# Kernel optimization log

Hardware: AMD Instinct MI355X
Metric: run time of the kernel (lower is better)

## Reference

```python
import jax, jax.numpy as jnp
import numpy as np

D_EMB, N_HEADS = 1024, 16
D_K = D_EMB // N_HEADS

def setup_inputs() -> dict:
    key = jax.random.key(0)
    ks = jax.random.split(key, 5)
    scale = 0.02
    return {
        "n": jax.random.normal(ks[0], (2, 2048, D_EMB), dtype=jnp.float32),
        "W_q": jax.random.normal(ks[1], (D_EMB, D_EMB), dtype=jnp.float32) * scale,
        "W_k": jax.random.normal(ks[2], (D_EMB, D_EMB), dtype=jnp.float32) * scale,
        "W_v": jax.random.normal(ks[3], (D_EMB, D_EMB), dtype=jnp.float32) * scale,
        "W_o": jax.random.normal(ks[4], (D_EMB, D_EMB), dtype=jnp.float32) * scale,
    }

def reference(n, W_q, W_k, W_v, W_o):
    B, S, _ = n.shape
    # torch Linear(bias=False): y = x @ W.T, W is [out, in]
    def proj(x, W):
        y = jnp.einsum('bsd,ed->bse', x, W)
        return y.reshape(B, S, N_HEADS, D_K).transpose(0, 2, 1, 3)  # [B,H,S,Dk]
    Q, K, V = proj(n, W_q), proj(n, W_k), proj(n, W_v)
    A = jnp.einsum('bhqd,bhkd->bhqk', Q, K) * (D_K ** -0.5)
    A = jnp.clip(A, -5.0, 5.0)
    A = jax.nn.softmax(A, axis=-1)
    ctx = jnp.einsum('bhqk,bhkd->bhqd', A, V)  # [B,H,S,Dk]
    ctx = ctx.transpose(0, 2, 1, 3).reshape(B, S, D_EMB)
    return jnp.einsum('bsd,ed->bse', ctx, W_o)
```

## Files before the change

### kernel.cpp

```cpp
#include <hip/hip_runtime.h>
#include <hip/hip_bf16.h>
#include <stdint.h>

typedef __attribute__((ext_vector_type(4))) float floatx4;
typedef __attribute__((ext_vector_type(8))) short shortx8;
typedef __attribute__((ext_vector_type(4))) unsigned short ushortx4;
typedef __attribute__((ext_vector_type(8))) unsigned short ushortx8;
typedef __attribute__((ext_vector_type(2))) uint32_t uintx2;

#define MFMA16(a, b, c) __builtin_amdgcn_mfma_f32_16x16x32_bf16((a), (b), (c), 0, 0, 0)

__device__ inline unsigned short f2bf(float f) {
    union { float f; uint32_t u; } v; v.f = f;
    uint32_t u = v.u;
    return (unsigned short)((u + 0x7FFFu + ((u >> 16) & 1u)) >> 16);
}

#if defined(__has_builtin) && __has_builtin(__builtin_amdgcn_cvt_pk_bf16_f32)
__device__ inline uint32_t pkbf(float a, float b) {
    auto r = __builtin_amdgcn_cvt_pk_bf16_f32(a, b);
    union { decltype(r) v; uint32_t u; } x; x.v = r; return x.u;
}
#else
__device__ inline uint32_t pkbf(float a, float b) {
    return ((uint32_t)f2bf(b) << 16) | f2bf(a);
}
#endif

#if defined(__has_builtin) && __has_builtin(__builtin_amdgcn_exp2f)
#define EXP2F(x) __builtin_amdgcn_exp2f(x)
#else
#define EXP2F(x) __expf((x) * 0.69314718056f)
#endif

__device__ inline void gl2lds16(const void* g, void* l) {
    __builtin_amdgcn_global_load_lds(
        (const __attribute__((address_space(1))) void*)(uintptr_t)g,
        (__attribute__((address_space(3))) void*)(uintptr_t)l, 16, 0, 0);
}

__global__ void convert_all(const float* __restrict__ n, const float* __restrict__ wq,
                            const float* __restrict__ wk, const float* __restrict__ wv,
                            const float* __restrict__ wo,
                            unsigned short* __restrict__ nb, unsigned short* __restrict__ wqb,
                            unsigned short* __restrict__ wkb, unsigned short* __restrict__ wvb,
                            unsigned short* __restrict__ wob) {
    int i = blockIdx.x * 256 + threadIdx.x;
    const float* src; unsigned short* dst; int off;
    if (i < 1048576) { src = n; dst = nb; off = i; }
    else {
        int j = i - 1048576; int r = j >> 18; int o = j & 262143;
        src = (r == 0) ? wq : (r == 1) ? wk : (r == 2) ? wv : wo;
        dst = (r == 0) ? wqb : (r == 1) ? wkb : (r == 2) ? wvb : wob;
        off = o;
    }
    floatx4 f = ((const floatx4*)src)[off];
    uintx2 u;
    u.x = pkbf(f.x, f.y); u.y = pkbf(f.z, f.w);
    ((uintx2*)dst)[off] = u;
}

__device__ inline void gemm_tile_128(const unsigned short* __restrict__ A,
                                     const unsigned short* __restrict__ B,
                                     unsigned short* sA, unsigned short* sB,
                                     floatx4 acc[4][4]) {
    const int tid = threadIdx.x, w = tid >> 6, l = tid & 63;
    const int c = l & 15, quad = l >> 4;
    const int wm = (w >> 1) * 64, wn = (w & 1) * 64;
    for (int kt = 0; kt < 16; ++kt) {
        #pragma unroll
        for (int r = 0; r < 4; ++r) {
            int row = r * 32 + w * 8 + (l >> 3);
            int cb  = (l & 7) ^ (row & 7);
            gl2lds16(A + row * 1024 + kt * 64 + cb * 8, (char*)sA + r * 4096 + w * 1024 + l * 16);
            gl2lds16(B + row * 1024 + kt * 64 + cb * 8, (char*)sB + r * 4096 + w * 1024 + l * 16);
        }
        __syncthreads();
        #pragma unroll
        for (int ks = 0; ks < 2; ++ks) {
            shortx8 af[4], bfr[4];
            #pragma unroll
            for (int i2 = 0; i2 < 4; ++i2) {
                int ra = wm + i2 * 16 + c;
                af[i2] = *(const shortx8*)((const char*)sA + ra * 128 + (((ks * 4 + quad) ^ (ra & 7)) * 16));
                int rb = wn + i2 * 16 + c;
                bfr[i2] = *(const shortx8*)((const char*)sB + rb * 128 + (((ks * 4 + quad) ^ (rb & 7)) * 16));
            }
            #pragma unroll
            for (int i2 = 0; i2 < 4; ++i2)
                #pragma unroll
                for (int j2 = 0; j2 < 4; ++j2)
                    acc[i2][j2] = MFMA16(af[i2], bfr[j2], acc[i2][j2]);
        }
        __syncthreads();
    }
}

__global__ void gemm_qkv(const unsigned short* __restrict__ nb,
                         const unsigned short* __restrict__ wqb,
                         const unsigned short* __restrict__ wkb,
                         const unsigned short* __restrict__ wvb,
                         unsigned short* __restrict__ Qb, unsigned short* __restrict__ Kb,
                         unsigned short* __restrict__ VTg) {
    __shared__ unsigned short sAB[2 * 128 * 64];
    unsigned short* sA = sAB;
    unsigned short* sB = sAB + 128 * 64;
    const int mt = blockIdx.x, nt = blockIdx.y;
    const int region = nt >> 3, nl0 = (nt & 7) * 128;
    const unsigned short* W = (region == 0) ? wqb : (region == 1) ? wkb : wvb;
    floatx4 acc[4][4] = {};
    gemm_tile_128(nb + mt * 128 * 1024, W + nl0 * 1024, sA, sB, acc);
    const int tid = threadIdx.x, w = tid >> 6, l = tid & 63, c = l & 15, quad = l >> 4;
    const int wm = (w >> 1) * 64, wn = (w & 1) * 64;
    if (region < 2) {
        unsigned short* O = (region == 0) ? Qb : Kb;
        const float sc = (region == 0) ? 0.18033688f : 1.0f;
        #pragma unroll
        for (int i2 = 0; i2 < 4; ++i2)
            #pragma unroll
            for (int j2 = 0; j2 < 4; ++j2)
                #pragma unroll
                for (int r = 0; r < 4; ++r) {
                    int row = wm + i2 * 16 + quad * 4 + r, col = wn + j2 * 16 + c;
                    sAB[row * 128 + col] = f2bf(acc[i2][j2][r] * sc);
                }
        __syncthreads();
        #pragma unroll
        for (int t = 0; t < 8; ++t) {
            int off = t * 4096 + tid * 16;
            int row = off >> 8, colb = off & 255;
            *(ushortx8*)((char*)(O + (mt * 128 + row) * 1024 + nl0) + colb) =
                *(const ushortx8*)((const char*)sAB + off);
        }
    } else {
        const int hh = w & 1, tt = w >> 1;
        char* img = (char*)sAB + (hh * 2 + tt) * 8192;
        #pragma unroll
        for (int i2 = 0; i2 < 4; ++i2)
            #pragma unroll
            for (int j2 = 0; j2 < 4; ++j2) {
                int d = j2 * 16 + c;
                int blk = (i2 >> 1) * 4 + quad;
                int phys = blk ^ (d & 7);
                uintx2 v;
                v.x = pkbf(acc[i2][j2][0], acc[i2][j2][1]);
                v.y = pkbf(acc[i2][j2][2], acc[i2][j2][3]);
                *(uintx2*)(img + d * 128 + phys * 16 + (i2 & 1) * 8) = v;
            }
        __syncthreads();
        const int h0 = (nt & 7) * 2, t0 = mt * 2;
        #pragma unroll
        for (int g = 0; g < 8; ++g) {
            int off = g * 4096 + tid * 16;
            int hsel = off >> 14, within = off & 16383;
            *(ushortx8*)((char*)VTg + (h0 + hsel) * 524288 + t0 * 8192 + within) =
                *(const ushortx8*)((const char*)sAB + off);
        }
    }
}

__global__ void __launch_bounds__(256) gemm_out(const unsigned short* __restrict__ ctx,
                         const unsigned short* __restrict__ wob,
                         float* __restrict__ out) {
    __shared__ unsigned short sA[128 * 64];
    __shared__ unsigned short sB[64 * 64];
    __shared__ float sC[64 * 64];
    const int mt = blockIdx.x, nt = blockIdx.y;
    const unsigned short* A = ctx + mt * 128 * 1024;
    const unsigned short* B = wob + nt * 64 * 1024;
    const int tid = threadIdx.x, w = tid >> 6, l = tid & 63, c = l & 15, quad = l >> 4;
    const int srow = w * 8 + (l >> 3), scb = l & 7;
    floatx4 acc[2][4] = {};
    for (int kt = 0; kt < 16; ++kt) {
        #pragma unroll
        for (int r = 0; r < 4; ++r) {
            int row = r * 32 + srow, cb = scb ^ (row & 7);
            gl2lds16(A + row * 1024 + kt * 64 + cb * 8, (char*)sA + r * 4096 + w * 1024 + l * 16);
        }
        #pragma unroll
        for (int r = 0; r < 2; ++r) {
            int row = r * 32 + srow, cb = scb ^ (row & 7);
            gl2lds16(B + row * 1024 + kt * 64 + cb * 8, (char*)sB + r * 4096 + w * 1024 + l * 16);
        }
        __syncthreads();
        #pragma unroll
        for (int ks = 0; ks < 2; ++ks) {
            shortx8 af[2], bf2[4];
            #pragma unroll
            for (int i2 = 0; i2 < 2; ++i2) {
                int ra = w * 32 + i2 * 16 + c;
                af[i2] = *(const shortx8*)((const char*)sA + ra * 128 + (((ks * 4 + quad) ^ (ra & 7)) * 16));
            }
            #pragma unroll
            for (int j2 = 0; j2 < 4; ++j2) {
                int rb = j2 * 16 + c;
                bf2[j2] = *(const shortx8*)((const char*)sB + rb * 128 + (((ks * 4 + quad) ^ (rb & 7)) * 16));
            }
            #pragma unroll
            for (int i2 = 0; i2 < 2; ++i2)
                #pragma unroll
                for (int j2 = 0; j2 < 4; ++j2)
                    acc[i2][j2] = MFMA16(af[i2], bf2[j2], acc[i2][j2]);
        }
        __syncthreads();
    }
    #pragma unroll
    for (int half = 0; half < 2; ++half) {
        if ((w >> 1) == half) {
            #pragma unroll
            for (int i2 = 0; i2 < 2; ++i2)
                #pragma unroll
                for (int j2 = 0; j2 < 4; ++j2)
                    #pragma unroll
                    for (int r = 0; r < 4; ++r) {
                        int row = (w & 1) * 32 + i2 * 16 + quad * 4 + r, col = j2 * 16 + c;
                        sC[row * 64 + col] = acc[i2][j2][r];
                    }
        }
        __syncthreads();
        #pragma unroll
        for (int t = 0; t < 4; ++t) {
            int off = t * 4096 + tid * 16;
            int row = off >> 8, colb = off & 255;
            *(floatx4*)((char*)(out + (mt * 128 + half * 64 + row) * 1024 + nt * 64) + colb) =
                *(const floatx4*)((const char*)sC + off);
        }
        __syncthreads();
    }
}

__global__ void __launch_bounds__(256, 2) attn(const unsigned short* __restrict__ Qb,
                     const unsigned short* __restrict__ Kb,
                     const unsigned short* __restrict__ VTg, unsigned short* __restrict__ ctx) {
    __shared__ char lds[81920];
    const int qt = blockIdx.x, h = blockIdx.y, b = blockIdx.z;
    const int tid = threadIdx.x, w = tid >> 6, l = tid & 63, c = l & 15, quad = l >> 4;
    const int tok0 = b * 2048 + qt * 128;
    const int srow = w * 8 + (l >> 3);
    const int cb = (l & 7) ^ (srow & 7);
    #pragma unroll
    for (int r = 0; r < 4; ++r)
        gl2lds16(Qb + (tok0 + r * 32 + srow) * 1024 + h * 64 + cb * 8, lds + r * 4096 + w * 1024 + l * 16);
    const unsigned short* Kbase = Kb + b * 2048 * 1024 + h * 64;
    const char* Vbase = (const char*)VTg + h * 524288 + (size_t)b * 262144;
    const char* Ksrc = (const char*)(Kbase + srow * 1024 + cb * 8);
    #define STAGE_K(kt, t) { _Pragma("unroll") for (int r = 0; r < 2; ++r) \
        gl2lds16(Ksrc + (size_t)(kt) * 131072 + r * 65536, lds + 16384 + (t) * 8192 + r * 4096 + w * 1024 + l * 16); }
    #define STAGE_V(kt, t) { _Pragma("unroll") for (int r = 0; r < 2; ++r) \
        gl2lds16(Vbase + (kt) * 8192 + r * 4096 + w * 1024 + l * 16, lds + 49152 + (t) * 8192 + r * 4096 + w * 1024 + l * 16); }
    STAGE_K(0, 0) STAGE_V(0, 0) STAGE_K(1, 1) STAGE_V(1, 1)
    __syncthreads();
    int lb[2];
    lb[0] = c * 128 + ((quad ^ (c & 7)) * 16);
    lb[1] = c * 128 + (((4 + quad) ^ (c & 7)) * 16);
    shortx8 qf[2][2];
    #pragma unroll
    for (int ks = 0; ks < 2; ++ks)
        #pragma unroll
        for (int qb = 0; qb < 2; ++qb)
            qf[ks][qb] = *(const shortx8*)(lds + (w * 2 + qb) * 2048 + lb[ks]);
    floatx4 cacc[4][2] = {};
    floatx4 sacc[2] = {};
    const shortx8 kone = {16256, 16256, 16256, 16256, 16256, 16256, 16256, 16256};
    const floatx4 fz = {0.f, 0.f, 0.f, 0.f};

    #define COMPUTE_S(t, s) { \
        shortx8 ak[4]; \
        _Pragma("unroll") for (int j = 0; j < 4; ++j) \
            ak[j] = *(const shortx8*)(lds + 16384 + (t) * 8192 + j * 2048 + lb[0]); \
        _Pragma("unroll") for (int j = 0; j < 4; ++j) \
            _Pragma("unroll") for (int qb = 0; qb < 2; ++qb) \
                s[qb][j] = MFMA16(ak[j], qf[0][qb], fz); \
        _Pragma("unroll") for (int j = 0; j < 4; ++j) \
            ak[j] = *(const shortx8*)(lds + 16384 + (t) * 8192 + j * 2048 + lb[1]); \
        _Pragma("unroll") for (int j = 0; j < 4; ++j) \
            _Pragma("unroll") for (int qb = 0; qb < 2; ++qb) \
                s[qb][j] = MFMA16(ak[j], qf[1][qb], s[qb][j]); }

    #define SOFTMAX_T(s) { _Pragma("unroll") for (int qb = 0; qb < 2; ++qb) \
        _Pragma("unroll") for (int j = 0; j < 4; ++j) \
            _Pragma("unroll") for (int r = 0; r < 4; ++r) \
                s[qb][j][r] = EXP2F(s[qb][j][r]); }

    #define PV_T(t, s) { _Pragma("unroll") for (int chunk = 0; chunk < 2; ++chunk) { \
        shortx8 av[4]; \
        _Pragma("unroll") for (int di = 0; di < 4; ++di) \
            av[di] = *(const shortx8*)(lds + 49152 + (t) * 8192 + di * 2048 + lb[chunk]); \
        shortx8 p[2]; \
        _Pragma("unroll") for (int qb = 0; qb < 2; ++qb) { \
            union { shortx8 v; uint32_t u[4]; } pk; \
            pk.u[0] = pkbf(s[qb][2 * chunk][0], s[qb][2 * chunk][1]); \
            pk.u[1] = pkbf(s[qb][2 * chunk][2], s[qb][2 * chunk][3]); \
            pk.u[2] = pkbf(s[qb][2 * chunk + 1][0], s[qb][2 * chunk + 1][1]); \
            pk.u[3] = pkbf(s[qb][2 * chunk + 1][2], s[qb][2 * chunk + 1][3]); \
            p[qb] = pk.v; \
            sacc[qb] = MFMA16(kone, p[qb], sacc[qb]); } \
        _Pragma("unroll") for (int di = 0; di < 4; ++di) \
            _Pragma("unroll") for (int qb = 0; qb < 2; ++qb) \
                cacc[di][qb] = MFMA16(av[di], p[qb], cacc[di][qb]); } }

    for (int p = 0; p < 16; ++p) {
        const int bufA = (p & 1) * 2, bufB = bufA + 1;
        if (p < 15) {
            const int nA = bufA ^ 2;
            STAGE_K(2 * p + 2, nA) STAGE_V(2 * p + 2, nA)
            STAGE_K(2 * p + 3, nA + 1) STAGE_V(2 * p + 3, nA + 1)
        }
        floatx4 sA[2][4], sB[2][4];
        COMPUTE_S(bufA, sA)
        COMPUTE_S(bufB, sB)
        SOFTMAX_T(sA)
        PV_T(bufA, sA)
        SOFTMAX_T(sB)
        PV_T(bufB, sB)
        if (p < 15) __syncthreads();
    }
    #pragma unroll
    for (int qb = 0; qb < 2; ++qb) {
        float inv = 1.0f / sacc[qb][0];
        int row = tok0 + w * 32 + qb * 16 + c;
        #pragma unroll
        for (int di = 0; di < 4; ++di) {
            uintx2 v;
            v.x = pkbf(cacc[di][qb][0] * inv, cacc[di][qb][1] * inv);
            v.y = pkbf(cacc[di][qb][2] * inv, cacc[di][qb][3] * inv);
            *(uintx2*)(ctx + row * 1024 + h * 64 + di * 16 + quad * 4) = v;
        }
    }
}

extern "C" void kernel_launch(void* const* d_in, const int* in_sizes, int n_in,
                              void* d_out, int out_size, void* d_ws, size_t ws_size,
                              hipStream_t stream) {
    const float* n  = (const float*)d_in[0];
    const float* wq = (const float*)d_in[1];
    const float* wk = (const float*)d_in[2];
    const float* wv = (const float*)d_in[3];
    const float* wo = (const float*)d_in[4];
    float* out = (float*)d_out;
    char* ws = (char*)d_ws;
    unsigned short* nb  = (unsigned short*)(ws);
    unsigned short* wqb = (unsigned short*)(ws + 8388608);
    unsigned short* wkb = (unsigned short*)(ws + 10485760);
    unsigned short* wvb = (unsigned short*)(ws + 12582912);
    unsigned short* wob = (unsigned short*)(ws + 14680064);
    unsigned short* Qb  = (unsigned short*)(ws + 16777216);
    unsigned short* Kb  = (unsigned short*)(ws + 25165824);
    unsigned short* VTg = (unsigned short*)(ws + 33554432);
    unsigned short* ctx = (unsigned short*)(ws + 41943040);

    convert_all<<<dim3(8192), dim3(256), 0, stream>>>(n, wq, wk, wv, wo, nb, wqb, wkb, wvb, wob);
    gemm_qkv<<<dim3(32, 24), dim3(256), 0, stream>>>(nb, wqb, wkb, wvb, Qb, Kb, VTg);
    attn<<<dim3(16, 16, 2), dim3(256), 0, stream>>>(Qb, Kb, VTg, ctx);
    gemm_out<<<dim3(32, 16), dim3(256), 0, stream>>>(ctx, wob, out);
}
```

Baseline: 171.3 us.

## Split attention work across 8 waves of 16 query rows, load Q directly

The attention kernel now runs 512 threads per block, with each wave handling 16 query rows instead of 32. K/V staging is spread across twice as many threads, so each thread issues one load per tile. Q fragments are read straight from global memory instead of through LDS, which shrinks LDS from 80KB to 64KB and cuts per-thread accumulator registers, aiming for higher occupancy and more latency hiding. In exchange each K/V tile in LDS is reused by fewer query rows per wave, so there are more LDS reads per MFMA.

```diff
diff --git a/kernel.cpp b/kernel.cpp
--- a/kernel.cpp
+++ b/kernel.cpp
@@ -229,75 +229,63 @@
     }
 }
 
-__global__ void __launch_bounds__(256, 2) attn(const unsigned short* __restrict__ Qb,
+__global__ void __launch_bounds__(512, 4) attn(const unsigned short* __restrict__ Qb,
                      const unsigned short* __restrict__ Kb,
                      const unsigned short* __restrict__ VTg, unsigned short* __restrict__ ctx) {
-    __shared__ char lds[81920];
+    __shared__ char lds[65536];
     const int qt = blockIdx.x, h = blockIdx.y, b = blockIdx.z;
     const int tid = threadIdx.x, w = tid >> 6, l = tid & 63, c = l & 15, quad = l >> 4;
     const int tok0 = b * 2048 + qt * 128;
-    const int srow = w * 8 + (l >> 3);
-    const int cb = (l & 7) ^ (srow & 7);
-    #pragma unroll
-    for (int r = 0; r < 4; ++r)
-        gl2lds16(Qb + (tok0 + r * 32 + srow) * 1024 + h * 64 + cb * 8, lds + r * 4096 + w * 1024 + l * 16);
-    const unsigned short* Kbase = Kb + b * 2048 * 1024 + h * 64;
+    const int srow = tid >> 3;
+    const int cb = (tid & 7) ^ (srow & 7);
+    const unsigned short* Kbase = Kb + (size_t)b * 2048 * 1024 + h * 64;
     const char* Vbase = (const char*)VTg + h * 524288 + (size_t)b * 262144;
     const char* Ksrc = (const char*)(Kbase + srow * 1024 + cb * 8);
-    #define STAGE_K(kt, t) { _Pragma("unroll") for (int r = 0; r < 2; ++r) \
-        gl2lds16(Ksrc + (size_t)(kt) * 131072 + r * 65536, lds + 16384 + (t) * 8192 + r * 4096 + w * 1024 + l * 16); }
-    #define STAGE_V(kt, t) { _Pragma("unroll") for (int r = 0; r < 2; ++r) \
-        gl2lds16(Vbase + (kt) * 8192 + r * 4096 + w * 1024 + l * 16, lds + 49152 + (t) * 8192 + r * 4096 + w * 1024 + l * 16); }
+    const int dst = w * 1024 + l * 16;
+    #define STAGE_K(kt, t) gl2lds16(Ksrc + (size_t)(kt) * 131072, lds + (t) * 8192 + dst);
+    #define STAGE_V(kt, t) gl2lds16(Vbase + (kt) * 8192 + tid * 16, lds + 32768 + (t) * 8192 + dst);
     STAGE_K(0, 0) STAGE_V(0, 0) STAGE_K(1, 1) STAGE_V(1, 1)
-    __syncthreads();
     int lb[2];
     lb[0] = c * 128 + ((quad ^ (c & 7)) * 16);
     lb[1] = c * 128 + (((4 + quad) ^ (c & 7)) * 16);
-    shortx8 qf[2][2];
+    shortx8 qf[2];
     #pragma unroll
     for (int ks = 0; ks < 2; ++ks)
-        #pragma unroll
-        for (int qb = 0; qb < 2; ++qb)
-            qf[ks][qb] = *(const shortx8*)(lds + (w * 2 + qb) * 2048 + lb[ks]);
-    floatx4 cacc[4][2] = {};
-    floatx4 sacc[2] = {};
+        qf[ks] = *(const shortx8*)(Qb + (tok0 + w * 16 + c) * 1024 + h * 64 + (ks * 4 + quad) * 8);
+    __syncthreads();
+    floatx4 cacc[4] = {};
+    floatx4 sacc = {};
     const shortx8 kone = {16256, 16256, 16256, 16256, 16256, 16256, 16256, 16256};
     const floatx4 fz = {0.f, 0.f, 0.f, 0.f};
 
     #define COMPUTE_S(t, s) { \
         shortx8 ak[4]; \
         _Pragma("unroll") for (int j = 0; j < 4; ++j) \
-            ak[j] = *(const shortx8*)(lds + 16384 + (t) * 8192 + j * 2048 + lb[0]); \
+            ak[j] = *(const shortx8*)(lds + (t) * 8192 + j * 2048 + lb[0]); \
         _Pragma("unroll") for (int j = 0; j < 4; ++j) \
-            _Pragma("unroll") for (int qb = 0; qb < 2; ++qb) \
-                s[qb][j] = MFMA16(ak[j], qf[0][qb], fz); \
+            s[j] = MFMA16(ak[j], qf[0], fz); \
         _Pragma("unroll") for (int j = 0; j < 4; ++j) \
-            ak[j] = *(const shortx8*)(lds + 16384 + (t) * 8192 + j * 2048 + lb[1]); \
+            ak[j] = *(const shortx8*)(lds + (t) * 8192 + j * 2048 + lb[1]); \
         _Pragma("unroll") for (int j = 0; j < 4; ++j) \
-            _Pragma("unroll") for (int qb = 0; qb < 2; ++qb) \
-                s[qb][j] = MFMA16(ak[j], qf[1][qb], s[qb][j]); }
-
-    #define SOFTMAX_T(s) { _Pragma("unroll") for (int qb = 0; qb < 2; ++qb) \
-        _Pragma("unroll") for (int j = 0; j < 4; ++j) \
+            s[j] = MFMA16(ak[j], qf[1], s[j]); }
+
+    #define SOFTMAX_T(s) { _Pragma("unroll") for (int j = 0; j < 4; ++j) \
             _Pragma("unroll") for (int r = 0; r < 4; ++r) \
-                s[qb][j][r] = EXP2F(s[qb][j][r]); }
+                s[j][r] = EXP2F(s[j][r]); }
 
     #define PV_T(t, s) { _Pragma("unroll") for (int chunk = 0; chunk < 2; ++chunk) { \
         shortx8 av[4]; \
         _Pragma("unroll") for (int di = 0; di < 4; ++di) \
-            av[di] = *(const shortx8*)(lds + 49152 + (t) * 8192 + di * 2048 + lb[chunk]); \
-        shortx8 p[2]; \
-        _Pragma("unroll") for (int qb = 0; qb < 2; ++qb) { \
-            union { shortx8 v; uint32_t u[4]; } pk; \
-            pk.u[0] = pkbf(s[qb][2 * chunk][0], s[qb][2 * chunk][1]); \
-            pk.u[1] = pkbf(s[qb][2 * chunk][2], s[qb][2 * chunk][3]); \
-            pk.u[2] = pkbf(s[qb][2 * chunk + 1][0], s[qb][2 * chunk + 1][1]); \
-            pk.u[3] = pkbf(s[qb][2 * chunk + 1][2], s[qb][2 * chunk + 1][3]); \
-            p[qb] = pk.v; \
-            sacc[qb] = MFMA16(kone, p[qb], sacc[qb]); } \
+            av[di] = *(const shortx8*)(lds + 32768 + (t) * 8192 + di * 2048 + lb[chunk]); \
+        union { shortx8 v; uint32_t u[4]; } pk; \
+        pk.u[0] = pkbf(s[2 * chunk][0], s[2 * chunk][1]); \
+        pk.u[1] = pkbf(s[2 * chunk][2], s[2 * chunk][3]); \
+        pk.u[2] = pkbf(s[2 * chunk + 1][0], s[2 * chunk + 1][1]); \
+        pk.u[3] = pkbf(s[2 * chunk + 1][2], s[2 * chunk + 1][3]); \
+        shortx8 p = pk.v; \
+        sacc = MFMA16(kone, p, sacc); \
         _Pragma("unroll") for (int di = 0; di < 4; ++di) \
-            _Pragma("unroll") for (int qb = 0; qb < 2; ++qb) \
-                cacc[di][qb] = MFMA16(av[di], p[qb], cacc[di][qb]); } }
+            cacc[di] = MFMA16(av[di], p, cacc[di]); } }
 
     for (int p = 0; p < 16; ++p) {
         const int bufA = (p & 1) * 2, bufB = bufA + 1;
@@ -306,7 +294,7 @@
             STAGE_K(2 * p + 2, nA) STAGE_V(2 * p + 2, nA)
             STAGE_K(2 * p + 3, nA + 1) STAGE_V(2 * p + 3, nA + 1)
         }
-        floatx4 sA[2][4], sB[2][4];
+        floatx4 sA[4], sB[4];
         COMPUTE_S(bufA, sA)
         COMPUTE_S(bufB, sB)
         SOFTMAX_T(sA)
@@ -315,15 +303,14 @@
         PV_T(bufB, sB)
         if (p < 15) __syncthreads();
     }
-    #pragma unroll
-    for (int qb = 0; qb < 2; ++qb) {
-        float inv = 1.0f / sacc[qb][0];
-        int row = tok0 + w * 32 + qb * 16 + c;
+    {
+        float inv = 1.0f / sacc[0];
+        int row = tok0 + w * 16 + c;
         #pragma unroll
         for (int di = 0; di < 4; ++di) {
             uintx2 v;
-            v.x = pkbf(cacc[di][qb][0] * inv, cacc[di][qb][1] * inv);
-            v.y = pkbf(cacc[di][qb][2] * inv, cacc[di][qb][3] * inv);
+            v.x = pkbf(cacc[di][0] * inv, cacc[di][1] * inv);
+            v.y = pkbf(cacc[di][2] * inv, cacc[di][3] * inv);
             *(uintx2*)(ctx + row * 1024 + h * 64 + di * 16 + quad * 4) = v;
         }
     }
@@ -351,6 +338,6 @@
 
     convert_all<<<dim3(8192), dim3(256), 0, stream>>>(n, wq, wk, wv, wo, nb, wqb, wkb, wvb, wob);
     gemm_qkv<<<dim3(32, 24), dim3(256), 0, stream>>>(nb, wqb, wkb, wvb, Qb, Kb, VTg);
-    attn<<<dim3(16, 16, 2), dim3(256), 0, stream>>>(Qb, Kb, VTg, ctx);
+    attn<<<dim3(16, 16, 2), dim3(512), 0, stream>>>(Qb, Kb, VTg, ctx);
     gemm_out<<<dim3(32, 16), dim3(256), 0, stream>>>(ctx, wob, out);
 }
```

Result: no change. 172.9 us (+0.9%).

## Split attention KV range across two wave groups per block with LDS reduction

Applied to the files above, without the earlier changes.

The attention kernel now launches 512 threads per block. Two groups of four waves each take alternate key tiles of the same query tile, and their unnormalized context and row sums are combined through LDS at the end. Q fragments are loaded straight from global memory instead of being staged in LDS, which cuts LDS use to 64KB. The aim is more waves per CU for latency hiding. The cost is an extra reduction step, and every thread's QK^T and PV work runs on half the keys.

```diff
diff --git a/kernel.cpp b/kernel.cpp
--- a/kernel.cpp
+++ b/kernel.cpp
@@ -229,50 +229,51 @@
     }
 }
 
-__global__ void __launch_bounds__(256, 2) attn(const unsigned short* __restrict__ Qb,
+__global__ void __launch_bounds__(512, 4) attn(const unsigned short* __restrict__ Qb,
                      const unsigned short* __restrict__ Kb,
                      const unsigned short* __restrict__ VTg, unsigned short* __restrict__ ctx) {
-    __shared__ char lds[81920];
+    __shared__ char lds[65536];
     const int qt = blockIdx.x, h = blockIdx.y, b = blockIdx.z;
     const int tid = threadIdx.x, w = tid >> 6, l = tid & 63, c = l & 15, quad = l >> 4;
+    const int g = w >> 2, wg = w & 3;
     const int tok0 = b * 2048 + qt * 128;
-    const int srow = w * 8 + (l >> 3);
-    const int cb = (l & 7) ^ (srow & 7);
-    #pragma unroll
-    for (int r = 0; r < 4; ++r)
-        gl2lds16(Qb + (tok0 + r * 32 + srow) * 1024 + h * 64 + cb * 8, lds + r * 4096 + w * 1024 + l * 16);
-    const unsigned short* Kbase = Kb + b * 2048 * 1024 + h * 64;
+    const int srow = tid >> 3;
+    const int cb = (tid & 7) ^ (srow & 7);
+    const unsigned short* Kbase = Kb + (size_t)b * 2048 * 1024 + h * 64;
     const char* Vbase = (const char*)VTg + h * 524288 + (size_t)b * 262144;
     const char* Ksrc = (const char*)(Kbase + srow * 1024 + cb * 8);
-    #define STAGE_K(kt, t) { _Pragma("unroll") for (int r = 0; r < 2; ++r) \
-        gl2lds16(Ksrc + (size_t)(kt) * 131072 + r * 65536, lds + 16384 + (t) * 8192 + r * 4096 + w * 1024 + l * 16); }
-    #define STAGE_V(kt, t) { _Pragma("unroll") for (int r = 0; r < 2; ++r) \
-        gl2lds16(Vbase + (kt) * 8192 + r * 4096 + w * 1024 + l * 16, lds + 49152 + (t) * 8192 + r * 4096 + w * 1024 + l * 16); }
+    const int dst = tid * 16;
+    #define STAGE_K(kt, t) gl2lds16(Ksrc + (size_t)(kt) * 131072, lds + (t) * 8192 + dst);
+    #define STAGE_V(kt, t) gl2lds16(Vbase + (kt) * 8192 + dst, lds + 32768 + (t) * 8192 + dst);
     STAGE_K(0, 0) STAGE_V(0, 0) STAGE_K(1, 1) STAGE_V(1, 1)
-    __syncthreads();
-    int lb[2];
-    lb[0] = c * 128 + ((quad ^ (c & 7)) * 16);
-    lb[1] = c * 128 + (((4 + quad) ^ (c & 7)) * 16);
+    const int lb0 = c * 128 + ((quad ^ (c & 7)) * 16);
+    const int lb1 = c * 128 + (((4 + quad) ^ (c & 7)) * 16);
+    const char* kA0 = lds + g * 8192 + lb0;
+    const char* kA1 = lds + g * 8192 + lb1;
+    const char* vA0 = lds + 32768 + g * 8192 + lb0;
+    const char* vA1 = lds + 32768 + g * 8192 + lb1;
     shortx8 qf[2][2];
     #pragma unroll
     for (int ks = 0; ks < 2; ++ks)
         #pragma unroll
         for (int qb = 0; qb < 2; ++qb)
-            qf[ks][qb] = *(const shortx8*)(lds + (w * 2 + qb) * 2048 + lb[ks]);
+            qf[ks][qb] = *(const shortx8*)(Qb + (size_t)(tok0 + wg * 32 + qb * 16 + c) * 1024
+                                              + h * 64 + (ks * 4 + quad) * 8);
+    __syncthreads();
     floatx4 cacc[4][2] = {};
     floatx4 sacc[2] = {};
     const shortx8 kone = {16256, 16256, 16256, 16256, 16256, 16256, 16256, 16256};
     const floatx4 fz = {0.f, 0.f, 0.f, 0.f};
 
-    #define COMPUTE_S(t, s) { \
+    #define COMPUTE_S(BOFF, s) { \
         shortx8 ak[4]; \
         _Pragma("unroll") for (int j = 0; j < 4; ++j) \
-            ak[j] = *(const shortx8*)(lds + 16384 + (t) * 8192 + j * 2048 + lb[0]); \
+            ak[j] = *(const shortx8*)(kA0 + (BOFF) + j * 2048); \
         _Pragma("unroll") for (int j = 0; j < 4; ++j) \
             _Pragma("unroll") for (int qb = 0; qb < 2; ++qb) \
                 s[qb][j] = MFMA16(ak[j], qf[0][qb], fz); \
         _Pragma("unroll") for (int j = 0; j < 4; ++j) \
-            ak[j] = *(const shortx8*)(lds + 16384 + (t) * 8192 + j * 2048 + lb[1]); \
+            ak[j] = *(const shortx8*)(kA1 + (BOFF) + j * 2048); \
         _Pragma("unroll") for (int j = 0; j < 4; ++j) \
             _Pragma("unroll") for (int qb = 0; qb < 2; ++qb) \
                 s[qb][j] = MFMA16(ak[j], qf[1][qb], s[qb][j]); }
@@ -282,10 +283,11 @@
             _Pragma("unroll") for (int r = 0; r < 4; ++r) \
                 s[qb][j][r] = EXP2F(s[qb][j][r]); }
 
-    #define PV_T(t, s) { _Pragma("unroll") for (int chunk = 0; chunk < 2; ++chunk) { \
+    #define PV_T(BOFF, s) { _Pragma("unroll") for (int chunk = 0; chunk < 2; ++chunk) { \
         shortx8 av[4]; \
+        const char* vb = chunk ? vA1 : vA0; \
         _Pragma("unroll") for (int di = 0; di < 4; ++di) \
-            av[di] = *(const shortx8*)(lds + 49152 + (t) * 8192 + di * 2048 + lb[chunk]); \
+            av[di] = *(const shortx8*)(vb + (BOFF) + di * 2048); \
         shortx8 p[2]; \
         _Pragma("unroll") for (int qb = 0; qb < 2; ++qb) { \
             union { shortx8 v; uint32_t u[4]; } pk; \
@@ -299,32 +301,56 @@
             _Pragma("unroll") for (int qb = 0; qb < 2; ++qb) \
                 cacc[di][qb] = MFMA16(av[di], p[qb], cacc[di][qb]); } }
 
-    for (int p = 0; p < 16; ++p) {
-        const int bufA = (p & 1) * 2, bufB = bufA + 1;
-        if (p < 15) {
-            const int nA = bufA ^ 2;
-            STAGE_K(2 * p + 2, nA) STAGE_V(2 * p + 2, nA)
-            STAGE_K(2 * p + 3, nA + 1) STAGE_V(2 * p + 3, nA + 1)
-        }
-        floatx4 sA[2][4], sB[2][4];
-        COMPUTE_S(bufA, sA)
-        COMPUTE_S(bufB, sB)
-        SOFTMAX_T(sA)
-        PV_T(bufA, sA)
-        SOFTMAX_T(sB)
-        PV_T(bufB, sB)
-        if (p < 15) __syncthreads();
-    }
-    #pragma unroll
-    for (int qb = 0; qb < 2; ++qb) {
-        float inv = 1.0f / sacc[qb][0];
-        int row = tok0 + w * 32 + qb * 16 + c;
-        #pragma unroll
-        for (int di = 0; di < 4; ++di) {
-            uintx2 v;
-            v.x = pkbf(cacc[di][qb][0] * inv, cacc[di][qb][1] * inv);
-            v.y = pkbf(cacc[di][qb][2] * inv, cacc[di][qb][3] * inv);
-            *(uintx2*)(ctx + row * 1024 + h * 64 + di * 16 + quad * 4) = v;
+    #define PHASE(p, BI, PREF) { \
+        if (PREF) { \
+            STAGE_K(2 * (p) + 2, (BI) ^ 2) STAGE_V(2 * (p) + 2, (BI) ^ 2) \
+            STAGE_K(2 * (p) + 3, ((BI) ^ 2) + 1) STAGE_V(2 * (p) + 3, ((BI) ^ 2) + 1) } \
+        floatx4 s[2][4]; \
+        COMPUTE_S((BI) * 8192, s) \
+        SOFTMAX_T(s) \
+        PV_T((BI) * 8192, s) \
+        if (PREF) __syncthreads(); }
+
+    for (int pp = 0; pp < 7; ++pp) {
+        PHASE(2 * pp, 0, 1)
+        PHASE(2 * pp + 1, 2, 1)
+    }
+    PHASE(14, 0, 1)
+    PHASE(15, 2, 0)
+
+    __syncthreads();
+    float* red = (float*)lds;
+    const int rbase = (wg * 64 + l) * 36;
+    if (g == 1) {
+        #pragma unroll
+        for (int qb = 0; qb < 2; ++qb)
+            #pragma unroll
+            for (int di = 0; di < 4; ++di)
+                *(floatx4*)(red + rbase + (qb * 4 + di) * 4) = cacc[di][qb];
+        red[rbase + 32] = sacc[0][0];
+        red[rbase + 33] = sacc[1][0];
+    }
+    __syncthreads();
+    if (g == 0) {
+        #pragma unroll
+        for (int qb = 0; qb < 2; ++qb)
+            #pragma unroll
+            for (int di = 0; di < 4; ++di)
+                cacc[di][qb] += *(const floatx4*)(red + rbase + (qb * 4 + di) * 4);
+        float invq[2];
+        invq[0] = 1.0f / (sacc[0][0] + red[rbase + 32]);
+        invq[1] = 1.0f / (sacc[1][0] + red[rbase + 33]);
+        #pragma unroll
+        for (int qb = 0; qb < 2; ++qb) {
+            float inv = invq[qb];
+            int row = tok0 + wg * 32 + qb * 16 + c;
+            #pragma unroll
+            for (int di = 0; di < 4; ++di) {
+                uintx2 v;
+                v.x = pkbf(cacc[di][qb][0] * inv, cacc[di][qb][1] * inv);
+                v.y = pkbf(cacc[di][qb][2] * inv, cacc[di][qb][3] * inv);
+                *(uintx2*)(ctx + row * 1024 + h * 64 + di * 16 + quad * 4) = v;
+            }
         }
     }
 }
@@ -351,6 +377,6 @@
 
     convert_all<<<dim3(8192), dim3(256), 0, stream>>>(n, wq, wk, wv, wo, nb, wqb, wkb, wvb, wob);
     gemm_qkv<<<dim3(32, 24), dim3(256), 0, stream>>>(nb, wqb, wkb, wvb, Qb, Kb, VTg);
-    attn<<<dim3(16, 16, 2), dim3(256), 0, stream>>>(Qb, Kb, VTg, ctx);
+    attn<<<dim3(16, 16, 2), dim3(512), 0, stream>>>(Qb, Kb, VTg, ctx);
     gemm_out<<<dim3(32, 16), dim3(256), 0, stream>>>(ctx, wob, out);
 }
```

Result: slower. 183.5 us (+7.2%).
